# Kernel optimization log

Measured on AMD Instinct MI355X. Metric: run time of the kernel, lower is better.

## Reference

```python
import jax, jax.numpy as jnp
import numpy as np

HEADS = 16
THETA = 10000.0


def _rope(x):
    # lucidrains rotary_embedding_torch, interleaved-pair convention, dim = full hidden size
    b, n, d = x.shape
    half = d // 2
    inv_freq = 1.0 / (THETA ** (jnp.arange(0, d, 2, dtype=jnp.float32) / d))  # (half,)
    ang = jnp.arange(n, dtype=jnp.float32)[:, None] * inv_freq               # (n, half)
    cos, sin = jnp.cos(ang), jnp.sin(ang)
    xp = x.reshape(b, n, half, 2)
    x1, x2 = xp[..., 0], xp[..., 1]
    out = jnp.stack([x1 * cos - x2 * sin, x2 * cos + x1 * sin], axis=-1)
    return out.reshape(b, n, d)


def setup_inputs() -> dict:
    key = jax.random.key(0)
    ks = jax.random.split(key, 8)
    B, N, C = 8, 2048, 1024
    s = C ** -0.5
    return {
        "x": jax.random.normal(ks[0], (B, N, C), jnp.float32),
        "Wq": jax.random.normal(ks[1], (C, C), jnp.float32) * s,
        "bq": jax.random.normal(ks[2], (C,), jnp.float32) * 0.01,
        "Wk": jax.random.normal(ks[3], (C, C), jnp.float32) * s,
        "bk": jax.random.normal(ks[4], (C,), jnp.float32) * 0.01,
        "Wv": jax.random.normal(ks[5], (C, C), jnp.float32) * s,
        "bv": jax.random.normal(ks[6], (C,), jnp.float32) * 0.01,
        "gamma": jnp.ones((C,), jnp.float32),
        "beta": jnp.zeros((C,), jnp.float32),
    }


def reference(x, Wq, bq, Wk, bk, Wv, bv, gamma, beta):
    b, n, c = x.shape
    h = HEADS
    d = c // h
    gelu = lambda t: jax.nn.gelu(t, approximate=False)  # torch nn.GELU default = exact erf

    q = gelu(x @ Wq.T + bq) + 0.21
    k = gelu(x @ Wk.T + bk) + 0.21
    v = x @ Wv.T + bv

    q_r = _rope(q)
    k_r = _rope(k)

    split = lambda t: t.reshape(b, n, h, d).transpose(0, 2, 1, 3)  # (b,h,n,d)
    qh, kh, vh, qrh, krh = split(q), split(k), split(v), split(q_r), split(k_r)

    # z = 1 / (q @ mean_n(k)^T + 1e-6), shape (b,h,n,1)
    z = 1.0 / (jnp.einsum('bhnd,bhd->bhn', qh, kh.mean(axis=2)) + 1e-6)

    # kv = (k_rope^T * n^-0.5) @ (v * n^-0.5) -> (b,h,d,d)
    scale = n ** (-0.5)
    kv = jnp.einsum('bhnd,bhne->bhde', krh * scale, vh * scale)

    out = jnp.einsum('bhnd,bhde->bhne', qrh, kv) * z[..., None]  # (b,h,n,d)
    out = out.transpose(0, 2, 1, 3).reshape(b, n, c)

    # dropout is identity at eval; residual + LayerNorm(eps=1e-12)
    res = out + x
    mu = res.mean(-1, keepdims=True)
    var = res.var(-1, keepdims=True)  # biased variance, matches torch LayerNorm
    return (res - mu) / jnp.sqrt(var + 1e-12) * gamma + beta
```

## Files before the change

kernel.cpp:

```cpp
#include <hip/hip_runtime.h>
#include <cstdint>
#include <cstddef>

#define NB 8
#define SEQ 2048
#define CH 1024
#define NH 16
#define HD 64
#define MROWS (NB*SEQ)
#define HALFC 512

typedef __attribute__((ext_vector_type(4))) float f32x4;
typedef __attribute__((ext_vector_type(8))) short s16x8;

__device__ __forceinline__ ushort f2bf(float f) {
    union { float f; unsigned u; } v; v.f = f;
    unsigned r = (v.u + 0x7FFFu + ((v.u >> 16) & 1u)) >> 16;
    return (ushort)r;
}
__device__ __forceinline__ float bf2f(ushort u) {
    union { unsigned u; float f; } v; v.u = ((unsigned)u) << 16;
    return v.f;
}
__device__ __forceinline__ void gload16(const ushort* g, ushort* l) {
    __builtin_amdgcn_global_load_lds((const __attribute__((address_space(1))) unsigned*)g,
                                     (__attribute__((address_space(3))) unsigned*)l, 16, 0, 0);
}

__device__ __forceinline__ float fast_erf(float x) {
    float ax = fabsf(x);
    float d = __fmaf_rn(0.3275911f, ax, 1.f);
    float t; asm("v_rcp_f32 %0, %1" : "=v"(t) : "v"(d));
    float p = __fmaf_rn(1.061405429f, t, -1.453152027f);
    p = __fmaf_rn(p, t, 1.421413741f);
    p = __fmaf_rn(p, t, -0.284496736f);
    p = __fmaf_rn(p, t, 0.254829592f);
    p = p * t;
    float e = __expf(-ax * ax);
    float r = 1.f - p * e;
    return copysignf(r, x);
}

__global__ void cvt_bf16_kernel(const float* __restrict__ src, ushort* __restrict__ dst, int n4) {
    int i = blockIdx.x * 256 + threadIdx.x;
    if (i >= n4) return;
    f32x4 v = ((const f32x4*)src)[i];
    ushort4 o;
    o.x = f2bf(v[0]); o.y = f2bf(v[1]); o.z = f2bf(v[2]); o.w = f2bf(v[3]);
    ((ushort4*)dst)[i] = o;
}

__global__ void rope_table_kernel(float2* __restrict__ csT) {
    int idx = blockIdx.x * 256 + threadIdx.x;
    int n = idx >> 9;
    int i = idx & 511;
    float freq = powf(10000.f, -(float)i * (1.f / 512.f));
    float a = (float)n * freq;
    float s, c;
    sincosf(a, &s, &c);
    csT[idx] = make_float2(c, s);
}

__global__ __launch_bounds__(256, 2) void qkv_gemm_kernel(
    const ushort* __restrict__ xb, const ushort* __restrict__ wb,
    const float* __restrict__ bq, const float* __restrict__ bk, const float* __restrict__ bv,
    const float2* __restrict__ csT,
    ushort* __restrict__ qr, ushort* __restrict__ kr, ushort* __restrict__ vo,
    float* __restrict__ ksum)
{
    __shared__ ushort As[128 * 64];
    __shared__ ushort Bs[128 * 64];
    const int z = blockIdx.z;
    const ushort* w = wb + (size_t)z * CH * CH;
    const float* bias = (z == 0) ? bq : (z == 1) ? bk : bv;
    ushort* dst = (z == 0) ? qr : (z == 1) ? kr : vo;
    const int bid = blockIdx.x + 8 * blockIdx.y;
    const int l = (bid & 7) * 128 + (bid >> 3);
    const int row0 = (l >> 3) * 128;
    const int col0 = (l & 7) * 128;
    const int tid = threadIdx.x;
    const int lane = tid & 63;
    const int wid = tid >> 6;
    const int wm = (wid >> 1) * 64;
    const int wn = (wid & 1) * 64;

    f32x4 acc[4][4] = {};

    for (int kt = 0; kt < CH; kt += 64) {
        __syncthreads();
        #pragma unroll
        for (int i = 0; i < 4; ++i) {
            int cl = i * 256 + tid;
            int r = cl >> 3, ci = cl & 7;
            int sci = ci ^ (r & 7);
            gload16(xb + (size_t)(row0 + r) * CH + kt + sci * 8, (ushort*)&As[cl * 8]);
            gload16(w  + (size_t)(col0 + r) * CH + kt + sci * 8, (ushort*)&Bs[cl * 8]);
        }
        asm volatile("s_waitcnt vmcnt(0)" ::: "memory");
        __syncthreads();
        #pragma unroll
        for (int ks = 0; ks < 2; ++ks) {
            s16x8 af[4], bfr[4];
            #pragma unroll
            for (int mi = 0; mi < 4; ++mi) {
                int r = wm + mi * 16 + (lane & 15);
                int ch = ((lane >> 4) + ks * 4) ^ (r & 7);
                af[mi] = *(const s16x8*)&As[r * 64 + ch * 8];
            }
            #pragma unroll
            for (int ni = 0; ni < 4; ++ni) {
                int r = wn + ni * 16 + (lane & 15);
                int ch = ((lane >> 4) + ks * 4) ^ (r & 7);
                bfr[ni] = *(const s16x8*)&Bs[r * 64 + ch * 8];
            }
            #pragma unroll
            for (int mi = 0; mi < 4; ++mi)
                #pragma unroll
                for (int ni = 0; ni < 4; ++ni)
                    acc[mi][ni] = __builtin_amdgcn_mfma_f32_16x16x32_bf16(af[mi], bfr[ni], acc[mi][ni], 0, 0, 0);
        }
    }

    const int bidx = row0 >> 11;
    #pragma unroll
    for (int ni = 0; ni < 4; ++ni) {
        const int cg = col0 + wn + ni * 16 + (lane & 15);
        const float bsv = bias[cg];
        float cs = 0.f;
        #pragma unroll
        for (int mi = 0; mi < 4; ++mi) {
            const int mbase = row0 + wm + mi * 16 + ((lane >> 4) << 2);
            #pragma unroll
            for (int r = 0; r < 4; ++r) {
                float t = acc[mi][ni][r] + bsv;
                float val;
                if (z == 2) {
                    val = t;
                } else {
                    val = 0.5f * t * (1.f + fast_erf(t * 0.70710678f)) + 0.21f;
                }
                if (z == 1) cs += val;
                if (z != 2) {
                    float p = __shfl_xor(val, 1);
                    int n = (mbase + r) & (SEQ - 1);
                    float2 cv = csT[n * HALFC + (cg >> 1)];
                    val = (cg & 1) ? (p * cv.y + val * cv.x) : (val * cv.x - p * cv.y);
                }
                dst[(size_t)(mbase + r) * CH + cg] = f2bf(val);
            }
        }
        if (z == 1) {
            cs += __shfl_xor(cs, 16);
            cs += __shfl_xor(cs, 32);
            if (lane < 16) atomicAdd(&ksum[bidx * CH + cg], cs);
        }
    }
}

__global__ void z_kernel(const ushort* __restrict__ qr, const float* __restrict__ ksum,
                         const float2* __restrict__ csT, float* __restrict__ zout)
{
    int idx = blockIdx.x * 256 + threadIdx.x;
    int h = idx & 15;
    int m = idx >> 4;
    int b = m >> 11;
    int n = m & (SEQ - 1);
    const ushort* qp = qr + (size_t)m * CH + h * HD;
    const float* kmp = ksum + b * CH + h * HD;
    const float2* cp = csT + (size_t)n * HALFC + h * 32;
    float dot = 0.f;
    #pragma unroll
    for (int i = 0; i < 32; ++i) {
        float2 cv = cp[i];
        float km0 = kmp[2 * i], km1 = kmp[2 * i + 1];
        float q0 = bf2f(qp[2 * i]), q1 = bf2f(qp[2 * i + 1]);
        dot += q0 * (km0 * cv.x - km1 * cv.y) + q1 * (km0 * cv.y + km1 * cv.x);
    }
    dot *= (1.f / 2048.f);
    zout[((size_t)(b * NH + h)) * SEQ + n] = 1.f / (dot + 1e-6f);
}

__global__ __launch_bounds__(256, 2) void kv_partial_kernel(
    const ushort* __restrict__ kr, const ushort* __restrict__ vo, float* __restrict__ kvp)
{
    const int blk = blockIdx.x;
    const int chunk = blk & 7;
    const int bh = blk >> 3;
    const int b = bh >> 4, h = bh & 15;
    __shared__ float ks[64 * 68];
    __shared__ float vs[64 * 68];
    const int tid = threadIdx.x;
    const int d0 = (tid >> 4) * 4;
    const int e0 = (tid & 15) * 4;
    float acc[4][4] = {};
    const size_t base = ((size_t)b * SEQ + chunk * 256) * CH + h * HD;
    const int lrow = tid >> 2;
    const int lcol = (tid & 3) * 16;

    for (int it = 0; it < 4; ++it) {
        __syncthreads();
        const ushort* gk = kr + base + (size_t)(it * 64 + lrow) * CH + lcol;
        const ushort* gv = vo + base + (size_t)(it * 64 + lrow) * CH + lcol;
        s16x8 ka = *(const s16x8*)gk, kb2 = *(const s16x8*)(gk + 8);
        s16x8 va = *(const s16x8*)gv, vb2 = *(const s16x8*)(gv + 8);
        #pragma unroll
        for (int seg = 0; seg < 2; ++seg) {
            s16x8 kk = seg ? kb2 : ka;
            s16x8 vv = seg ? vb2 : va;
            #pragma unroll
            for (int q = 0; q < 2; ++q) {
                f32x4 tk, tv;
                #pragma unroll
                for (int e = 0; e < 4; ++e) {
                    tk[e] = bf2f((ushort)kk[q * 4 + e]);
                    tv[e] = bf2f((ushort)vv[q * 4 + e]);
                }
                *(f32x4*)&ks[lrow * 68 + lcol + seg * 8 + q * 4] = tk;
                *(f32x4*)&vs[lrow * 68 + lcol + seg * 8 + q * 4] = tv;
            }
        }
        __syncthreads();
        for (int n = 0; n < 64; ++n) {
            f32x4 kq = *(const f32x4*)&ks[n * 68 + d0];
            f32x4 vq = *(const f32x4*)&vs[n * 68 + e0];
            #pragma unroll
            for (int di = 0; di < 4; ++di)
                #pragma unroll
                for (int ej = 0; ej < 4; ++ej)
                    acc[di][ej] += kq[di] * vq[ej];
        }
    }
    float* op = kvp + (size_t)blk * 4096;
    #pragma unroll
    for (int di = 0; di < 4; ++di) {
        f32x4 t;
        t[0] = acc[di][0]; t[1] = acc[di][1]; t[2] = acc[di][2]; t[3] = acc[di][3];
        *(f32x4*)&op[(d0 + di) * 64 + e0] = t;
    }
}

__global__ void kv_reduce_kernel(const float* __restrict__ kvp, ushort* __restrict__ kvT) {
    int idx = blockIdx.x * 256 + threadIdx.x;
    int bh = idx >> 12;
    int de = idx & 4095;
    int e = de >> 6, d = de & 63;
    float s = 0.f;
    #pragma unroll
    for (int c = 0; c < 8; ++c)
        s += kvp[((size_t)bh * 8 + c) * 4096 + d * 64 + e];
    kvT[idx] = f2bf(s * (1.f / 2048.f));
}

__global__ __launch_bounds__(256, 2) void pv_kernel(
    const ushort* __restrict__ qr, const ushort* __restrict__ kvT,
    const float* __restrict__ zin, ushort* __restrict__ o)
{
    __shared__ ushort As[128 * 64];
    __shared__ ushort Bs[64 * 64];
    const int bh = blockIdx.y;
    const int b = bh >> 4, h = bh & 15;
    const int row0 = blockIdx.x * 128;
    const int tid = threadIdx.x;
    const int lane = tid & 63, wid = tid >> 6;
    const size_t grow = (size_t)b * SEQ + row0;

    #pragma unroll
    for (int i = 0; i < 4; ++i) {
        int cl = i * 256 + tid;
        int r = cl >> 3, ci = cl & 7;
        int sci = ci ^ (r & 7);
        gload16(qr + (grow + r) * CH + h * HD + sci * 8, (ushort*)&As[cl * 8]);
    }
    #pragma unroll
    for (int i = 0; i < 2; ++i) {
        int cl = i * 256 + tid;
        int r = cl >> 3, ci = cl & 7;
        int sci = ci ^ (r & 7);
        gload16(kvT + (size_t)bh * 4096 + r * 64 + sci * 8, (ushort*)&Bs[cl * 8]);
    }
    asm volatile("s_waitcnt vmcnt(0)" ::: "memory");
    __syncthreads();

    f32x4 acc[2][4] = {};
    #pragma unroll
    for (int ks2 = 0; ks2 < 2; ++ks2) {
        s16x8 af[2], bfr[4];
        #pragma unroll
        for (int mi = 0; mi < 2; ++mi) {
            int r = wid * 32 + mi * 16 + (lane & 15);
            int ch = ((lane >> 4) + ks2 * 4) ^ (r & 7);
            af[mi] = *(const s16x8*)&As[r * 64 + ch * 8];
        }
        #pragma unroll
        for (int ni = 0; ni < 4; ++ni) {
            int e = ni * 16 + (lane & 15);
            int ch = ((lane >> 4) + ks2 * 4) ^ (e & 7);
            bfr[ni] = *(const s16x8*)&Bs[e * 64 + ch * 8];
        }
        #pragma unroll
        for (int mi = 0; mi < 2; ++mi)
            #pragma unroll
            for (int ni = 0; ni < 4; ++ni)
                acc[mi][ni] = __builtin_amdgcn_mfma_f32_16x16x32_bf16(af[mi], bfr[ni], acc[mi][ni], 0, 0, 0);
    }

    const float* zp = zin + (size_t)bh * SEQ + row0;
    #pragma unroll
    for (int mi = 0; mi < 2; ++mi) {
        int mb = wid * 32 + mi * 16 + ((lane >> 4) << 2);
        #pragma unroll
        for (int r = 0; r < 4; ++r) {
            float zv = zp[mb + r];
            #pragma unroll
            for (int ni = 0; ni < 4; ++ni) {
                int e = ni * 16 + (lane & 15);
                o[(grow + mb + r) * CH + h * HD + e] = f2bf(acc[mi][ni][r] * zv);
            }
        }
    }
}

__global__ __launch_bounds__(256) void ln_kernel(
    const ushort* __restrict__ o, const float* __restrict__ x,
    const float* __restrict__ gamma, const float* __restrict__ beta,
    float* __restrict__ out)
{
    const int row = blockIdx.x;
    const int tid = threadIdx.x;
    const size_t base = (size_t)row * CH + tid * 4;
    f32x4 xv = *(const f32x4*)(x + base);
    ushort4 ov = *(const ushort4*)(o + base);
    float v0 = bf2f(ov.x) + xv[0];
    float v1 = bf2f(ov.y) + xv[1];
    float v2 = bf2f(ov.z) + xv[2];
    float v3 = bf2f(ov.w) + xv[3];
    float s = v0 + v1 + v2 + v3;
    float q = v0 * v0 + v1 * v1 + v2 * v2 + v3 * v3;
    #pragma unroll
    for (int off = 1; off < 64; off <<= 1) {
        s += __shfl_xor(s, off);
        q += __shfl_xor(q, off);
    }
    __shared__ float red[8];
    int wv = tid >> 6;
    if ((tid & 63) == 0) { red[wv] = s; red[4 + wv] = q; }
    __syncthreads();
    s = red[0] + red[1] + red[2] + red[3];
    q = red[4] + red[5] + red[6] + red[7];
    float mean = s * (1.f / 1024.f);
    float var = q * (1.f / 1024.f) - mean * mean;
    float rstd = rsqrtf(var + 1e-12f);
    f32x4 gv = *(const f32x4*)(gamma + tid * 4);
    f32x4 bv = *(const f32x4*)(beta + tid * 4);
    f32x4 res;
    res[0] = (v0 - mean) * rstd * gv[0] + bv[0];
    res[1] = (v1 - mean) * rstd * gv[1] + bv[1];
    res[2] = (v2 - mean) * rstd * gv[2] + bv[2];
    res[3] = (v3 - mean) * rstd * gv[3] + bv[3];
    *(f32x4*)(out + base) = res;
}

extern "C" void kernel_launch(void* const* d_in, const int* in_sizes, int n_in,
                              void* d_out, int out_size, void* d_ws, size_t ws_size,
                              hipStream_t stream) {
    const float* x     = (const float*)d_in[0];
    const float* Wq    = (const float*)d_in[1];
    const float* bq    = (const float*)d_in[2];
    const float* Wk    = (const float*)d_in[3];
    const float* bk    = (const float*)d_in[4];
    const float* Wv    = (const float*)d_in[5];
    const float* bv    = (const float*)d_in[6];
    const float* gamma = (const float*)d_in[7];
    const float* beta  = (const float*)d_in[8];
    float* out = (float*)d_out;
    char* ws = (char*)d_ws;

    ushort* xb   = (ushort*)(ws);
    ushort* wb   = (ushort*)(ws + (size_t)32 * 1048576);
    float2* csT  = (float2*)(ws + (size_t)38 * 1048576);
    ushort* qr   = (ushort*)(ws + (size_t)46  * 1048576);
    ushort* kr   = (ushort*)(ws + (size_t)78  * 1048576);
    ushort* vo   = (ushort*)(ws + (size_t)110 * 1048576);
    float*  ksum = (float*) (ws + (size_t)142 * 1048576);
    ushort* kvT  = (ushort*)(ws + (size_t)143 * 1048576);
    float*  zbuf = (float*) (ws + (size_t)144 * 1048576);
    float*  kvp  = (float*) (ws + (size_t)145 * 1048576);
    ushort* o    = xb;

    hipMemsetAsync(ksum, 0, NB * CH * sizeof(float), stream);
    cvt_bf16_kernel<<<16384, 256, 0, stream>>>(x, xb, MROWS * CH / 4);
    cvt_bf16_kernel<<<1024, 256, 0, stream>>>(Wq, wb,                 CH * CH / 4);
    cvt_bf16_kernel<<<1024, 256, 0, stream>>>(Wk, wb + CH * CH,       CH * CH / 4);
    cvt_bf16_kernel<<<1024, 256, 0, stream>>>(Wv, wb + 2 * CH * CH,   CH * CH / 4);
    rope_table_kernel<<<SEQ * HALFC / 256, 256, 0, stream>>>(csT);
    qkv_gemm_kernel<<<dim3(8, 128, 3), 256, 0, stream>>>(xb, wb, bq, bk, bv, csT, qr, kr, vo, ksum);
    z_kernel<<<MROWS * NH / 256, 256, 0, stream>>>(qr, ksum, csT, zbuf);
    kv_partial_kernel<<<NB * NH * 8, 256, 0, stream>>>(kr, vo, kvp);
    kv_reduce_kernel<<<NB * NH * 4096 / 256, 256, 0, stream>>>(kvp, kvT);
    pv_kernel<<<dim3(16, 128), 256, 0, stream>>>(qr, kvT, zbuf, o);
    ln_kernel<<<MROWS, 256, 0, stream>>>(o, x, gamma, beta, out);
}
```

Baseline: 422.8 us.

## Fuse z normalizer computation into pv kernel and raise GEMM occupancy bound

Drops the separate z_kernel and computes each row's 1/(q·mean_k + eps) inside pv_kernel from the q tile already staged in shared memory, storing it in a small shared array. This removes one launch and a full extra read of qr plus the zbuf round trip. It also raises the qkv GEMM launch_bounds occupancy hint from 2 to 4, which may force register spilling, and replaces powf with exp2f in the rope table. The price is an extra block barrier and some scalar work in pv_kernel.

```diff
diff --git a/kernel.cpp b/kernel.cpp
--- a/kernel.cpp
+++ b/kernel.cpp
@@ -54,14 +54,14 @@
     int idx = blockIdx.x * 256 + threadIdx.x;
     int n = idx >> 9;
     int i = idx & 511;
-    float freq = powf(10000.f, -(float)i * (1.f / 512.f));
+    float freq = exp2f((float)i * (-13.287712379549449f / 512.f));
     float a = (float)n * freq;
     float s, c;
     sincosf(a, &s, &c);
     csT[idx] = make_float2(c, s);
 }
 
-__global__ __launch_bounds__(256, 2) void qkv_gemm_kernel(
+__global__ __launch_bounds__(256, 4) void qkv_gemm_kernel(
     const ushort* __restrict__ xb, const ushort* __restrict__ wb,
     const float* __restrict__ bq, const float* __restrict__ bk, const float* __restrict__ bv,
     const float2* __restrict__ csT,
@@ -157,29 +157,6 @@
     }
 }
 
-__global__ void z_kernel(const ushort* __restrict__ qr, const float* __restrict__ ksum,
-                         const float2* __restrict__ csT, float* __restrict__ zout)
-{
-    int idx = blockIdx.x * 256 + threadIdx.x;
-    int h = idx & 15;
-    int m = idx >> 4;
-    int b = m >> 11;
-    int n = m & (SEQ - 1);
-    const ushort* qp = qr + (size_t)m * CH + h * HD;
-    const float* kmp = ksum + b * CH + h * HD;
-    const float2* cp = csT + (size_t)n * HALFC + h * 32;
-    float dot = 0.f;
-    #pragma unroll
-    for (int i = 0; i < 32; ++i) {
-        float2 cv = cp[i];
-        float km0 = kmp[2 * i], km1 = kmp[2 * i + 1];
-        float q0 = bf2f(qp[2 * i]), q1 = bf2f(qp[2 * i + 1]);
-        dot += q0 * (km0 * cv.x - km1 * cv.y) + q1 * (km0 * cv.y + km1 * cv.x);
-    }
-    dot *= (1.f / 2048.f);
-    zout[((size_t)(b * NH + h)) * SEQ + n] = 1.f / (dot + 1e-6f);
-}
-
 __global__ __launch_bounds__(256, 2) void kv_partial_kernel(
     const ushort* __restrict__ kr, const ushort* __restrict__ vo, float* __restrict__ kvp)
 {
@@ -253,10 +230,12 @@
 
 __global__ __launch_bounds__(256, 2) void pv_kernel(
     const ushort* __restrict__ qr, const ushort* __restrict__ kvT,
-    const float* __restrict__ zin, ushort* __restrict__ o)
+    const float* __restrict__ ksum, const float2* __restrict__ csT,
+    ushort* __restrict__ o)
 {
     __shared__ ushort As[128 * 64];
     __shared__ ushort Bs[64 * 64];
+    __shared__ float zrow[128];
     const int bh = blockIdx.y;
     const int b = bh >> 4, h = bh & 15;
     const int row0 = blockIdx.x * 128;
@@ -281,6 +260,30 @@
     asm volatile("s_waitcnt vmcnt(0)" ::: "memory");
     __syncthreads();
 
+    {
+        const int r = tid >> 1, hh = tid & 1;
+        const int n = row0 + r;
+        const float* kmp = ksum + b * CH + h * HD + hh * 32;
+        const float2* cp = csT + (size_t)n * HALFC + h * 32 + hh * 16;
+        float part = 0.f;
+        #pragma unroll
+        for (int cc = 0; cc < 4; ++cc) {
+            int chunk = hh * 4 + cc;
+            s16x8 qv = *(const s16x8*)&As[r * 64 + (chunk ^ (r & 7)) * 8];
+            #pragma unroll
+            for (int j = 0; j < 4; ++j) {
+                float q0 = bf2f((ushort)qv[2 * j]);
+                float q1 = bf2f((ushort)qv[2 * j + 1]);
+                float km0 = kmp[cc * 8 + 2 * j];
+                float km1 = kmp[cc * 8 + 2 * j + 1];
+                float2 cv = cp[cc * 4 + j];
+                part += q0 * (km0 * cv.x - km1 * cv.y) + q1 * (km0 * cv.y + km1 * cv.x);
+            }
+        }
+        part += __shfl_xor(part, 1);
+        if (hh == 0) zrow[r] = 1.f / (part * (1.f / 2048.f) + 1e-6f);
+    }
+
     f32x4 acc[2][4] = {};
     #pragma unroll
     for (int ks2 = 0; ks2 < 2; ++ks2) {
@@ -304,13 +307,14 @@
                 acc[mi][ni] = __builtin_amdgcn_mfma_f32_16x16x32_bf16(af[mi], bfr[ni], acc[mi][ni], 0, 0, 0);
     }
 
-    const float* zp = zin + (size_t)bh * SEQ + row0;
+    __syncthreads();
+
     #pragma unroll
     for (int mi = 0; mi < 2; ++mi) {
         int mb = wid * 32 + mi * 16 + ((lane >> 4) << 2);
         #pragma unroll
         for (int r = 0; r < 4; ++r) {
-            float zv = zp[mb + r];
+            float zv = zrow[mb + r];
             #pragma unroll
             for (int ni = 0; ni < 4; ++ni) {
                 int e = ni * 16 + (lane & 15);
@@ -383,7 +387,6 @@
     ushort* vo   = (ushort*)(ws + (size_t)110 * 1048576);
     float*  ksum = (float*) (ws + (size_t)142 * 1048576);
     ushort* kvT  = (ushort*)(ws + (size_t)143 * 1048576);
-    float*  zbuf = (float*) (ws + (size_t)144 * 1048576);
     float*  kvp  = (float*) (ws + (size_t)145 * 1048576);
     ushort* o    = xb;
 
@@ -394,9 +397,8 @@
     cvt_bf16_kernel<<<1024, 256, 0, stream>>>(Wv, wb + 2 * CH * CH,   CH * CH / 4);
     rope_table_kernel<<<SEQ * HALFC / 256, 256, 0, stream>>>(csT);
     qkv_gemm_kernel<<<dim3(8, 128, 3), 256, 0, stream>>>(xb, wb, bq, bk, bv, csT, qr, kr, vo, ksum);
-    z_kernel<<<MROWS * NH / 256, 256, 0, stream>>>(qr, ksum, csT, zbuf);
     kv_partial_kernel<<<NB * NH * 8, 256, 0, stream>>>(kr, vo, kvp);
     kv_reduce_kernel<<<NB * NH * 4096 / 256, 256, 0, stream>>>(kvp, kvT);
-    pv_kernel<<<dim3(16, 128), 256, 0, stream>>>(qr, kvT, zbuf, o);
+    pv_kernel<<<dim3(16, 128), 256, 0, stream>>>(qr, kvT, ksum, csT, o);
     ln_kernel<<<MROWS, 256, 0, stream>>>(o, x, gamma, beta, out);
 }
```

Result: faster. 402.7 us (-4.8%).
